# Kernel optimization log

Measured on AMD Instinct MI355X. Metric: run time of the kernel, lower is better.

The kernel has to match this reference:

```python
import jax, jax.numpy as jnp
import numpy as np

N, C, H, W = 4, 64, 64, 64
EPS = 1e-5


def setup_inputs() -> dict:
    key = jax.random.key(0)
    ks = jax.random.split(key, 8)
    f = lambda k, s: jax.random.normal(k, s, dtype=jnp.float32)
    return {
        "low_feats": f(ks[0], (N, C, H, W)),
        "heat0": f(ks[1], (N, C, H, W)),
        "heat1": f(ks[2], (N, C, H, W)),
        # f_query: 1x1 conv + BN(gamma,beta) + ReLU
        "Wq": f(ks[3], (C, C)) * 0.05, "bq": jnp.zeros((C,), jnp.float32),
        "gq": jnp.ones((C,), jnp.float32), "betaq": jnp.zeros((C,), jnp.float32),
        # f_key: 1x1 conv + BN + ReLU
        "Wk": f(ks[4], (C, C)) * 0.05, "bk": jnp.zeros((C,), jnp.float32),
        "gk": jnp.ones((C,), jnp.float32), "betak": jnp.zeros((C,), jnp.float32),
        # f_value: plain 1x1 conv
        "Wv": f(ks[5], (C, C)) * 0.05, "bv": jnp.zeros((C,), jnp.float32),
    }


def _conv1x1(x, Wc, bc):
    # [N,C,H,W] -> [N,O,H,W]
    return jnp.einsum("oc,nchw->nohw", Wc, x) + bc[None, :, None, None]


def _conv_bn_relu(x, Wc, bc, g, beta):
    y = _conv1x1(x, Wc, bc)
    mu = y.mean(axis=(0, 2, 3), keepdims=True)      # batch-stat BN (train mode)
    var = y.var(axis=(0, 2, 3), keepdims=True)
    y = (y - mu) * jax.lax.rsqrt(var + EPS)
    y = y * g[None, :, None, None] + beta[None, :, None, None]
    return jax.nn.relu(y)


def reference(low_feats, heat0, heat1, Wq, bq, gq, betaq, Wk, bk, gk, betak, Wv, bv):
    n, c, h, w = low_feats.shape
    hw = h * w
    query = _conv_bn_relu(low_feats, Wq, bq, gq, betaq).reshape(n, c, hw).transpose(0, 2, 1)  # [N,HW,C]
    keym = _conv_bn_relu(low_feats, Wk, bk, gk, betak).reshape(n, c, hw)                      # [N,C,HW]
    value = _conv1x1(low_feats, Wv, bv).reshape(n, c, hw).transpose(0, 2, 1)                  # [N,HW,C]
    sim = jax.nn.softmax(jnp.einsum("nqc,nck->nqk", query, keym), axis=-1)                    # [N,HW,HW]
    # dual gated value paths share the softmax map: sim@vI + sim@vC == sim@(vI+vC)
    gate = (heat0 + heat1).reshape(n, c, hw).transpose(0, 2, 1)                               # [N,HW,C]
    gated_v = gate * value
    ctx = jnp.einsum("nqk,nkc->nqc", sim, gated_v)                                            # [N,HW,C]
    return ctx.transpose(0, 2, 1).reshape(n, c, h, w)
```

## Files before the change

### kernel.cpp

```cpp
#include <hip/hip_runtime.h>

#define NB 4
#define CC 64
#define HW 4096
#define NT (NB*HW)
#define EPSV 1e-5f
#define LOG2E 1.4426950408889634f

typedef _Float16 f16;
typedef _Float16 half4 __attribute__((ext_vector_type(4)));
typedef _Float16 half8 __attribute__((ext_vector_type(8)));
typedef float   float4v __attribute__((ext_vector_type(4)));

#define NELEM ((size_t)NB*HW*CC)

#define PART_OFF 512
#define TEN_OFF  264192

__global__ __launch_bounds__(512)
void conv2_kernel(const float* __restrict__ x,
                  const float* __restrict__ h0, const float* __restrict__ h1,
                  const float* __restrict__ Wq, const float* __restrict__ bq,
                  const float* __restrict__ Wk, const float* __restrict__ bk,
                  const float* __restrict__ Wv, const float* __restrict__ bv,
                  float* __restrict__ ws,
                  f16* __restrict__ q, f16* __restrict__ k, f16* __restrict__ gv)
{
    __shared__ float Wl[3][32*CC];
    __shared__ float xs[CC][64];
    const int t   = threadIdx.x;
    const int n   = blockIdx.y;
    const int z   = blockIdx.z;
    const int px0 = blockIdx.x * 64;
    const int px  = t & 63;
    const int grp = t >> 6;
    const int ocl = grp * 4;
    const int oc0 = z*32 + ocl;

    ((float4*)Wl[0])[t] = ((const float4*)(Wq + (size_t)z*32*CC))[t];
    ((float4*)Wl[1])[t] = ((const float4*)(Wk + (size_t)z*32*CC))[t];
    ((float4*)Wl[2])[t] = ((const float4*)(Wv + (size_t)z*32*CC))[t];
    for (int i = t; i < CC*64; i += 512) {
        int ic = i >> 6, p = i & 63;
        xs[ic][p] = x[((size_t)n*CC + ic)*HW + px0 + p];
    }
    __syncthreads();

    float aq[4], ak[4], av[4];
    #pragma unroll
    for (int j = 0; j < 4; ++j) { aq[j] = bq[oc0+j]; ak[j] = bk[oc0+j]; av[j] = bv[oc0+j]; }

    for (int ic = 0; ic < CC; ic += 4) {
        float xv0 = xs[ic  ][px];
        float xv1 = xs[ic+1][px];
        float xv2 = xs[ic+2][px];
        float xv3 = xs[ic+3][px];
        #pragma unroll
        for (int j = 0; j < 4; ++j) {
            const int row = (ocl+j)*CC + ic;
            float4 wq = *(const float4*)&Wl[0][row];
            float4 wk = *(const float4*)&Wl[1][row];
            float4 wv = *(const float4*)&Wl[2][row];
            aq[j] = fmaf(wq.x,xv0, fmaf(wq.y,xv1, fmaf(wq.z,xv2, fmaf(wq.w,xv3, aq[j]))));
            ak[j] = fmaf(wk.x,xv0, fmaf(wk.y,xv1, fmaf(wk.z,xv2, fmaf(wk.w,xv3, ak[j]))));
            av[j] = fmaf(wv.x,xv0, fmaf(wv.y,xv1, fmaf(wv.z,xv2, fmaf(wv.w,xv3, av[j]))));
        }
    }

    const size_t base = ((size_t)n*HW + px0 + px)*CC + oc0;
    half4 vq, vk;
    #pragma unroll
    for (int j = 0; j < 4; ++j) { vq[j] = (f16)aq[j]; vk[j] = (f16)ak[j]; }
    *(half4*)&q[base] = vq;
    *(half4*)&k[base] = vk;

    #pragma unroll
    for (int j = 0; j < 4; ++j) {
        size_t gi = ((size_t)n*CC + oc0 + j)*HW + px0 + px;
        gv[gi] = (f16)((h0[gi] + h1[gi]) * av[j]);
    }

    float* slot = ws + PART_OFF + (size_t)(n*(HW/64) + blockIdx.x)*256;
    #pragma unroll
    for (int j = 0; j < 4; ++j) {
        float v0 = aq[j], v1 = aq[j]*aq[j], v2 = ak[j], v3 = ak[j]*ak[j];
        #pragma unroll
        for (int off = 32; off > 0; off >>= 1) {
            v0 += __shfl_down(v0, off);
            v1 += __shfl_down(v1, off);
            v2 += __shfl_down(v2, off);
            v3 += __shfl_down(v3, off);
        }
        if (px == 0) {
            slot[      oc0 + j] = v0;
            slot[ 64 + oc0 + j] = v1;
            slot[128 + oc0 + j] = v2;
            slot[192 + oc0 + j] = v3;
        }
    }
}

__global__ __launch_bounds__(256)
void bnstats_kernel(const float* __restrict__ gq, const float* __restrict__ betaq,
                    const float* __restrict__ gk, const float* __restrict__ betak,
                    float* __restrict__ ws)
{
    __shared__ float tot[256];
    const int i = threadIdx.x;
    float acc = 0.0f;
    #pragma unroll 8
    for (int b = 0; b < 256; ++b) acc += ws[PART_OFF + b*256 + i];
    tot[i] = acc;
    __syncthreads();

    if (i < 64) {
        float mean = tot[i] * (1.0f / NT);
        float var  = tot[64 + i] * (1.0f / NT) - mean*mean;
        float s    = gq[i] * rsqrtf(var + EPSV);
        ws[256 + i] = s;
        ws[320 + i] = betaq[i] - mean*s;
    } else if (i < 128) {
        int c = i - 64;
        float mean = tot[128 + c] * (1.0f / NT);
        float var  = tot[192 + c] * (1.0f / NT) - mean*mean;
        float s    = gk[c] * rsqrtf(var + EPSV);
        ws[384 + c] = s * LOG2E;
        ws[448 + c] = (betak[c] - mean*s) * LOG2E;
    }
}

__global__ __launch_bounds__(256)
void apply_kernel(f16* __restrict__ q, f16* __restrict__ k,
                  const float* __restrict__ ws)
{
    __shared__ float sc[CC], sh[CC];
    const int t = threadIdx.x;
    const int tens = blockIdx.y;
    if (t < 64)       sc[t]    = ws[256 + tens*128 + t];
    else if (t < 128) sh[t-64] = ws[320 + tens*128 + (t-64)];
    __syncthreads();

    f16* p = tens ? k : q;
    const size_t e0 = ((size_t)blockIdx.x * 256 + t) * 8;
    const int c0 = (int)(e0 & 63);

    half8 v = *(half8*)&p[e0];
    half8 o;
    #pragma unroll
    for (int j = 0; j < 8; ++j)
        o[j] = (f16)fmaxf(fmaf(sc[c0+j], (float)v[j], sh[c0+j]), 0.0f);
    *(half8*)&p[e0] = o;
}

__global__ __launch_bounds__(512, 2)
void attn_kernel(const f16* __restrict__ q, const f16* __restrict__ k,
                 const f16* __restrict__ gv, float* __restrict__ out)
{
    __shared__ float Obuf[8][4][256];
    __shared__ float MLbuf[2][8][64];

    const int t    = threadIdx.x;
    const int n    = blockIdx.y;
    const int w    = t >> 6;
    const int lane = t & 63;
    const int m16  = lane & 15;
    const int kb   = lane >> 4;
    const int q0   = blockIdx.x * 64;

    half8 qf[4][2];
    #pragma unroll
    for (int qt = 0; qt < 4; ++qt) {
        const size_t qb = ((size_t)n*HW + q0 + qt*16 + m16)*CC + kb*8;
        qf[qt][0] = *(const half8*)&q[qb];
        qf[qt][1] = *(const half8*)&q[qb + 32];
    }

    const int    kt0   = w * 512;
    const size_t krow  = (size_t)n*HW*CC;
    const size_t gbase = ((size_t)n*CC + m16)*HW;

    half8 khf[2][2][2];
    half4 gvf[2][2][4];

#define LOADK(B, KT) do {                                                     \
    size_t a_ = krow + ((size_t)(KT) + m16)*CC + kb*8;                        \
    khf[B][0][0] = *(const half8*)&k[a_];                                     \
    khf[B][0][1] = *(const half8*)&k[a_ + 32];                                \
    khf[B][1][0] = *(const half8*)&k[a_ + 16*CC];                             \
    khf[B][1][1] = *(const half8*)&k[a_ + 16*CC + 32];                        \
} while (0)

#define LOADGV(B, KT) do {                                                    \
    size_t g_ = gbase + (size_t)(KT) + kb*4;                                  \
    _Pragma("unroll") for (int k2_ = 0; k2_ < 2; ++k2_)                       \
    _Pragma("unroll") for (int ct_ = 0; ct_ < 4; ++ct_)                       \
        gvf[B][k2_][ct_] = *(const half4*)&gv[g_ + k2_*16 + (size_t)ct_*16*HW];\
} while (0)

    float4v accO[4][4];
    #pragma unroll
    for (int qt = 0; qt < 4; ++qt)
        #pragma unroll
        for (int ct = 0; ct < 4; ++ct) accO[qt][ct] = (float4v){0.f,0.f,0.f,0.f};
    float m[4] = {-INFINITY,-INFINITY,-INFINITY,-INFINITY};
    float l[4] = {0.f,0.f,0.f,0.f};

#define STEP(B, NB_, KTN) do {                                                \
    LOADK(NB_, KTN);                                                          \
    LOADGV(NB_, KTN);                                                         \
    float4v accS[4][2];                                                       \
    _Pragma("unroll") for (int qt_ = 0; qt_ < 4; ++qt_)                       \
    _Pragma("unroll") for (int k2_ = 0; k2_ < 2; ++k2_) {                     \
        float4v z_ = {0.f,0.f,0.f,0.f};                                       \
        z_ = __builtin_amdgcn_mfma_f32_16x16x32_f16(khf[B][k2_][0], qf[qt_][0], z_, 0,0,0); \
        accS[qt_][k2_] = __builtin_amdgcn_mfma_f32_16x16x32_f16(khf[B][k2_][1], qf[qt_][1], z_, 0,0,0); \
    }                                                                         \
    _Pragma("unroll") for (int qt_ = 0; qt_ < 4; ++qt_) {                     \
        float mx = fmaxf(fmaxf(fmaxf(accS[qt_][0][0], accS[qt_][0][1]),       \
                               fmaxf(accS[qt_][0][2], accS[qt_][0][3])),      \
                         fmaxf(fmaxf(accS[qt_][1][0], accS[qt_][1][1]),       \
                               fmaxf(accS[qt_][1][2], accS[qt_][1][3])));     \
        mx = fmaxf(mx, __shfl_xor(mx, 16));                                   \
        mx = fmaxf(mx, __shfl_xor(mx, 32));                                   \
        float mn = fmaxf(m[qt_], mx);                                         \
        float al = exp2f(m[qt_] - mn);  m[qt_] = mn;                          \
        float p0 = exp2f(accS[qt_][0][0]-mn), p1 = exp2f(accS[qt_][0][1]-mn); \
        float p2 = exp2f(accS[qt_][0][2]-mn), p3 = exp2f(accS[qt_][0][3]-mn); \
        float p4 = exp2f(accS[qt_][1][0]-mn), p5 = exp2f(accS[qt_][1][1]-mn); \
        float p6 = exp2f(accS[qt_][1][2]-mn), p7 = exp2f(accS[qt_][1][3]-mn); \
        l[qt_] = fmaf(l[qt_], al, ((p0+p1)+(p2+p3)) + ((p4+p5)+(p6+p7)));     \
        half4 pfa, pfb;                                                       \
        pfa[0]=(f16)p0; pfa[1]=(f16)p1; pfa[2]=(f16)p2; pfa[3]=(f16)p3;       \
        pfb[0]=(f16)p4; pfb[1]=(f16)p5; pfb[2]=(f16)p6; pfb[3]=(f16)p7;       \
        _Pragma("unroll") for (int ct_ = 0; ct_ < 4; ++ct_) {                 \
            float4v o_ = accO[qt_][ct_];                                      \
            o_[0]*=al; o_[1]*=al; o_[2]*=al; o_[3]*=al;                       \
            o_ = __builtin_amdgcn_mfma_f32_16x16x16f16(gvf[B][0][ct_], pfa, o_, 0,0,0); \
            accO[qt_][ct_] = __builtin_amdgcn_mfma_f32_16x16x16f16(gvf[B][1][ct_], pfb, o_, 0,0,0); \
        }                                                                     \
    }                                                                         \
} while (0)

    LOADK(0, kt0);
    LOADGV(0, kt0);
    for (int i2 = 0; i2 < 8; ++i2) {
        const int kA = kt0 + i2*64;
        STEP(0, 1, kA + 32);
        STEP(1, 0, kA + 64);
    }

    #pragma unroll
    for (int qt = 0; qt < 4; ++qt) {
        l[qt] += __shfl_xor(l[qt], 16);
        l[qt] += __shfl_xor(l[qt], 32);
    }
    if (kb == 0) {
        #pragma unroll
        for (int qt = 0; qt < 4; ++qt) {
            MLbuf[0][w][qt*16 + m16] = m[qt];
            MLbuf[1][w][qt*16 + m16] = l[qt];
        }
    }
    __syncthreads();

    float invL[4];
    #pragma unroll
    for (int qt = 0; qt < 4; ++qt) {
        const int r = qt*16 + m16;
        float M = MLbuf[0][0][r];
        #pragma unroll
        for (int src = 1; src < 8; ++src) M = fmaxf(M, MLbuf[0][src][r]);
        float L = 0.0f;
        #pragma unroll
        for (int src = 0; src < 8; ++src)
            L += MLbuf[1][src][r] * exp2f(MLbuf[0][src][r] - M);
        const float f = exp2f(m[qt] - M);
        #pragma unroll
        for (int ct = 0; ct < 4; ++ct) {
            accO[qt][ct][0] *= f; accO[qt][ct][1] *= f;
            accO[qt][ct][2] *= f; accO[qt][ct][3] *= f;
        }
        invL[qt] = 1.0f / L;
    }

    for (int rd = 0; rd < 4; ++rd) {
        __syncthreads();
        #pragma unroll
        for (int ct = 0; ct < 4; ++ct)
            ((float4*)&Obuf[w][ct][0])[lane] =
                (float4){accO[rd][ct][0], accO[rd][ct][1], accO[rd][ct][2], accO[rd][ct][3]};
        __syncthreads();
        if (w < 4) {
            float4 s = ((float4*)&Obuf[0][w][0])[lane];
            #pragma unroll
            for (int src = 1; src < 8; ++src) {
                float4 v = ((float4*)&Obuf[src][w][0])[lane];
                s.x += v.x; s.y += v.y; s.z += v.z; s.w += v.w;
            }
            const float iv = invL[rd];
            const int chb = w*16 + kb*4;
            const int row = q0 + rd*16 + m16;
            out[((size_t)n*CC + chb + 0)*HW + row] = s.x * iv;
            out[((size_t)n*CC + chb + 1)*HW + row] = s.y * iv;
            out[((size_t)n*CC + chb + 2)*HW + row] = s.z * iv;
            out[((size_t)n*CC + chb + 3)*HW + row] = s.w * iv;
        }
    }
#undef STEP
#undef LOADGV
#undef LOADK
}

extern "C" void kernel_launch(void* const* d_in, const int* in_sizes, int n_in,
                              void* d_out, int out_size, void* d_ws, size_t ws_size,
                              hipStream_t stream)
{
    const float* low   = (const float*)d_in[0];
    const float* h0    = (const float*)d_in[1];
    const float* h1    = (const float*)d_in[2];
    const float* Wq    = (const float*)d_in[3];
    const float* bq    = (const float*)d_in[4];
    const float* gq    = (const float*)d_in[5];
    const float* betaq = (const float*)d_in[6];
    const float* Wk    = (const float*)d_in[7];
    const float* bk    = (const float*)d_in[8];
    const float* gk    = (const float*)d_in[9];
    const float* betak = (const float*)d_in[10];
    const float* Wv    = (const float*)d_in[11];
    const float* bv    = (const float*)d_in[12];

    float* wsf = (float*)d_ws;
    float* out = (float*)d_out;

    f16* q  = (f16*)((char*)d_ws + TEN_OFF);
    f16* k  = q + NELEM;
    f16* gv = k + NELEM;

    conv2_kernel<<<dim3(HW/64, NB, 2), 512, 0, stream>>>(
        low, h0, h1, Wq, bq, Wk, bk, Wv, bv, wsf, q, k, gv);

    bnstats_kernel<<<1, 256, 0, stream>>>(gq, betaq, gk, betak, wsf);

    apply_kernel<<<dim3((int)(NELEM/(256*8)), 2), 256, 0, stream>>>(q, k, wsf);

    attn_kernel<<<dim3(HW/64, NB), 512, 0, stream>>>(q, k, gv, out);
}
```

Before: 182.2 us.

## Skip softmax rescale when max unchanged, compute row sums via MFMA, split conv finer

Result: faster. 164.6 us (-9.7%).

```diff
diff --git a/kernel.cpp b/kernel.cpp
--- a/kernel.cpp
+++ b/kernel.cpp
@@ -17,7 +17,7 @@
 #define PART_OFF 512
 #define TEN_OFF  264192
 
-__global__ __launch_bounds__(512)
+__global__ __launch_bounds__(256)
 void conv2_kernel(const float* __restrict__ x,
                   const float* __restrict__ h0, const float* __restrict__ h1,
                   const float* __restrict__ Wq, const float* __restrict__ bq,
@@ -26,7 +26,7 @@
                   float* __restrict__ ws,
                   f16* __restrict__ q, f16* __restrict__ k, f16* __restrict__ gv)
 {
-    __shared__ float Wl[3][32*CC];
+    __shared__ float Wl[3][16*CC];
     __shared__ float xs[CC][64];
     const int t   = threadIdx.x;
     const int n   = blockIdx.y;
@@ -35,12 +35,12 @@
     const int px  = t & 63;
     const int grp = t >> 6;
     const int ocl = grp * 4;
-    const int oc0 = z*32 + ocl;
-
-    ((float4*)Wl[0])[t] = ((const float4*)(Wq + (size_t)z*32*CC))[t];
-    ((float4*)Wl[1])[t] = ((const float4*)(Wk + (size_t)z*32*CC))[t];
-    ((float4*)Wl[2])[t] = ((const float4*)(Wv + (size_t)z*32*CC))[t];
-    for (int i = t; i < CC*64; i += 512) {
+    const int oc0 = z*16 + ocl;
+
+    ((float4*)Wl[0])[t] = ((const float4*)(Wq + (size_t)z*16*CC))[t];
+    ((float4*)Wl[1])[t] = ((const float4*)(Wk + (size_t)z*16*CC))[t];
+    ((float4*)Wl[2])[t] = ((const float4*)(Wv + (size_t)z*16*CC))[t];
+    for (int i = t; i < CC*64; i += 256) {
         int ic = i >> 6, p = i & 63;
         xs[ic][p] = x[((size_t)n*CC + ic)*HW + px0 + p];
     }
@@ -181,6 +181,7 @@
 
     half8 khf[2][2][2];
     half4 gvf[2][2][4];
+    const half4 ones = {(f16)1.f, (f16)1.f, (f16)1.f, (f16)1.f};
 
 #define LOADK(B, KT) do {                                                     \
     size_t a_ = krow + ((size_t)(KT) + m16)*CC + kb*8;                        \
@@ -197,13 +198,14 @@
         gvf[B][k2_][ct_] = *(const half4*)&gv[g_ + k2_*16 + (size_t)ct_*16*HW];\
 } while (0)
 
-    float4v accO[4][4];
-    #pragma unroll
-    for (int qt = 0; qt < 4; ++qt)
+    float4v accO[4][4], accL[4];
+    #pragma unroll
+    for (int qt = 0; qt < 4; ++qt) {
         #pragma unroll
         for (int ct = 0; ct < 4; ++ct) accO[qt][ct] = (float4v){0.f,0.f,0.f,0.f};
+        accL[qt] = (float4v){0.f,0.f,0.f,0.f};
+    }
     float m[4] = {-INFINITY,-INFINITY,-INFINITY,-INFINITY};
-    float l[4] = {0.f,0.f,0.f,0.f};
 
 #define STEP(B, NB_, KTN) do {                                                \
     LOADK(NB_, KTN);                                                          \
@@ -215,26 +217,43 @@
         z_ = __builtin_amdgcn_mfma_f32_16x16x32_f16(khf[B][k2_][0], qf[qt_][0], z_, 0,0,0); \
         accS[qt_][k2_] = __builtin_amdgcn_mfma_f32_16x16x32_f16(khf[B][k2_][1], qf[qt_][1], z_, 0,0,0); \
     }                                                                         \
+    float mx[4];                                                              \
     _Pragma("unroll") for (int qt_ = 0; qt_ < 4; ++qt_) {                     \
-        float mx = fmaxf(fmaxf(fmaxf(accS[qt_][0][0], accS[qt_][0][1]),       \
+        float v_ = fmaxf(fmaxf(fmaxf(accS[qt_][0][0], accS[qt_][0][1]),       \
                                fmaxf(accS[qt_][0][2], accS[qt_][0][3])),      \
                          fmaxf(fmaxf(accS[qt_][1][0], accS[qt_][1][1]),       \
                                fmaxf(accS[qt_][1][2], accS[qt_][1][3])));     \
-        mx = fmaxf(mx, __shfl_xor(mx, 16));                                   \
-        mx = fmaxf(mx, __shfl_xor(mx, 32));                                   \
-        float mn = fmaxf(m[qt_], mx);                                         \
-        float al = exp2f(m[qt_] - mn);  m[qt_] = mn;                          \
-        float p0 = exp2f(accS[qt_][0][0]-mn), p1 = exp2f(accS[qt_][0][1]-mn); \
-        float p2 = exp2f(accS[qt_][0][2]-mn), p3 = exp2f(accS[qt_][0][3]-mn); \
-        float p4 = exp2f(accS[qt_][1][0]-mn), p5 = exp2f(accS[qt_][1][1]-mn); \
-        float p6 = exp2f(accS[qt_][1][2]-mn), p7 = exp2f(accS[qt_][1][3]-mn); \
-        l[qt_] = fmaf(l[qt_], al, ((p0+p1)+(p2+p3)) + ((p4+p5)+(p6+p7)));     \
+        v_ = fmaxf(v_, __shfl_xor(v_, 16));                                   \
+        v_ = fmaxf(v_, __shfl_xor(v_, 32));                                   \
+        mx[qt_] = v_;                                                         \
+    }                                                                         \
+    int need_ = (mx[0] > m[0]) | (mx[1] > m[1]) |                             \
+                (mx[2] > m[2]) | (mx[3] > m[3]);                              \
+    if (__any(need_)) {                                                       \
+        _Pragma("unroll") for (int qt_ = 0; qt_ < 4; ++qt_) {                 \
+            float mn_ = fmaxf(m[qt_], mx[qt_]);                               \
+            float al_ = exp2f(m[qt_] - mn_);                                  \
+            m[qt_] = mn_;                                                     \
+            accL[qt_][0]*=al_; accL[qt_][1]*=al_;                             \
+            accL[qt_][2]*=al_; accL[qt_][3]*=al_;                             \
+            _Pragma("unroll") for (int ct_ = 0; ct_ < 4; ++ct_) {             \
+                accO[qt_][ct_][0]*=al_; accO[qt_][ct_][1]*=al_;               \
+                accO[qt_][ct_][2]*=al_; accO[qt_][ct_][3]*=al_;               \
+            }                                                                 \
+        }                                                                     \
+    }                                                                         \
+    _Pragma("unroll") for (int qt_ = 0; qt_ < 4; ++qt_) {                     \
+        float p0 = exp2f(accS[qt_][0][0]-m[qt_]), p1 = exp2f(accS[qt_][0][1]-m[qt_]); \
+        float p2 = exp2f(accS[qt_][0][2]-m[qt_]), p3 = exp2f(accS[qt_][0][3]-m[qt_]); \
+        float p4 = exp2f(accS[qt_][1][0]-m[qt_]), p5 = exp2f(accS[qt_][1][1]-m[qt_]); \
+        float p6 = exp2f(accS[qt_][1][2]-m[qt_]), p7 = exp2f(accS[qt_][1][3]-m[qt_]); \
         half4 pfa, pfb;                                                       \
         pfa[0]=(f16)p0; pfa[1]=(f16)p1; pfa[2]=(f16)p2; pfa[3]=(f16)p3;       \
         pfb[0]=(f16)p4; pfb[1]=(f16)p5; pfb[2]=(f16)p6; pfb[3]=(f16)p7;       \
+        accL[qt_] = __builtin_amdgcn_mfma_f32_16x16x16f16(ones, pfa, accL[qt_], 0,0,0); \
+        accL[qt_] = __builtin_amdgcn_mfma_f32_16x16x16f16(ones, pfb, accL[qt_], 0,0,0); \
         _Pragma("unroll") for (int ct_ = 0; ct_ < 4; ++ct_) {                 \
             float4v o_ = accO[qt_][ct_];                                      \
-            o_[0]*=al; o_[1]*=al; o_[2]*=al; o_[3]*=al;                       \
             o_ = __builtin_amdgcn_mfma_f32_16x16x16f16(gvf[B][0][ct_], pfa, o_, 0,0,0); \
             accO[qt_][ct_] = __builtin_amdgcn_mfma_f32_16x16x16f16(gvf[B][1][ct_], pfb, o_, 0,0,0); \
         }                                                                     \
@@ -249,16 +268,11 @@
         STEP(1, 0, kA + 64);
     }
 
-    #pragma unroll
-    for (int qt = 0; qt < 4; ++qt) {
-        l[qt] += __shfl_xor(l[qt], 16);
-        l[qt] += __shfl_xor(l[qt], 32);
-    }
     if (kb == 0) {
         #pragma unroll
         for (int qt = 0; qt < 4; ++qt) {
             MLbuf[0][w][qt*16 + m16] = m[qt];
-            MLbuf[1][w][qt*16 + m16] = l[qt];
+            MLbuf[1][w][qt*16 + m16] = accL[qt][0];
         }
     }
     __syncthreads();
@@ -336,7 +350,7 @@
     f16* k  = q + NELEM;
     f16* gv = k + NELEM;
 
-    conv2_kernel<<<dim3(HW/64, NB, 2), 512, 0, stream>>>(
+    conv2_kernel<<<dim3(HW/64, NB, 4), 256, 0, stream>>>(
         low, h0, h1, Wq, bq, Wk, bk, Wv, bv, wsf, q, k, gv);
 
     bnstats_kernel<<<1, 256, 0, stream>>>(gq, betaq, gk, betak, wsf);
```
